# Optimization experiments

Hardware: AMD Instinct MI355X
Metric: run time of the kernel (lower is better)

Reference implementation:

```python
import jax, jax.numpy as jnp
import numpy as np


def setup_inputs() -> dict:
    key = jax.random.key(0)
    B, T = 16384, 768
    inputs = jax.random.normal(key, (B, T, 2), dtype=jnp.float32)
    p = {"capacitance_x": 0.4, "capacitance_y": 0.4}
    for d in ["ax", "by", "xx", "xy", "yx", "yy"]:
        p[f"conductance_{d}"] = 0.001
        p[f"mean_{d}"] = 0.3
        p[f"std_{d}"] = 3.0
        p[f"pot_{d}"] = -1.0 if d in ("xy", "yx") else 1.0
    params = {k: jnp.full((1,), v, dtype=jnp.float32) for k, v in p.items()}
    return {"inputs": inputs, **params}


def reference(inputs, capacitance_x, capacitance_y,
              conductance_ax, mean_ax, std_ax, pot_ax,
              conductance_by, mean_by, std_by, pot_by,
              conductance_xx, mean_xx, std_xx, pot_xx,
              conductance_xy, mean_xy, std_xy, pot_xy,
              conductance_yx, mean_yx, std_yx, pot_yx,
              conductance_yy, mean_yy, std_yy, pot_yy):
    # inputs: [B, T, 2]; scan over T with carried state [B, 2]
    def syn(g, s, m, p, pre, post):
        # conductance * sigmoid(std*(pre-mean)) * (pot - post)
        return g * jax.nn.sigmoid(s * (pre - m)) * (p - post)

    def step(carry, inp):
        x, y = carry[:, :1], carry[:, 1:]          # [B,1] each
        a, b = inp[:, :1], inp[:, 1:]              # [B,1] each
        ix = (syn(conductance_ax, std_ax, mean_ax, pot_ax, a, x)
              + syn(conductance_xx, std_xx, mean_xx, pot_xx, x, x)
              + syn(conductance_yx, std_yx, mean_yx, pot_yx, y, x))
        iy = (syn(conductance_by, std_by, mean_by, pot_by, b, y)
              + syn(conductance_yy, std_yy, mean_yy, pot_yy, y, y)
              + syn(conductance_xy, std_xy, mean_xy, pot_xy, x, y))
        x = x + ix / capacitance_x
        y = y + iy / capacitance_y
        return jnp.concatenate([x, y], axis=-1), x

    B = inputs.shape[0]
    init = jnp.zeros((B, 2), dtype=inputs.dtype)
    _, ys = jax.lax.scan(step, init, jnp.swapaxes(inputs, 0, 1))  # ys: [T,B,1]
    return jnp.swapaxes(ys, 0, 1)  # [B,T,1]
```

## Files before the change

### kernel.cpp

```cpp
#include <hip/hip_runtime.h>

#define T_LEN 768
#define TC 32
#define NCH (T_LEN / TC)
#define RPB 32
#define RS  66
#define OS  66

struct Params { const float* p[27]; };

__device__ __forceinline__ float ex2(float x){ float r; asm("v_exp_f32 %0, %1":"=v"(r):"v"(x)); return r; }
__device__ __forceinline__ float frcp(float x){ return __builtin_amdgcn_rcpf(x); }
__device__ __forceinline__ float dpp_xor1(float x){
    return __int_as_float(__builtin_amdgcn_mov_dpp(__float_as_int(x),0xB1,0xF,0xF,true));
}
__device__ __forceinline__ float psig(float v, float k, float c){
    return frcp(1.0f + ex2(__builtin_fmaf(-k, v, c)));
}
__device__ __forceinline__ void wave_barrier(){
    asm volatile("s_waitcnt lgkmcnt(0)" ::: "memory");
    __builtin_amdgcn_s_barrier();
}

__global__ __launch_bounds__(192, 1) void cell_kernel(Params P, float* __restrict__ out) {
    __shared__ float r1buf[2][TC][RS];
    __shared__ float lds_o[2][TC][OS];

    const int tid = (int)threadIdx.x;
    const int r0  = (int)blockIdx.x * RPB;
    const int wv  = tid >> 6;
    const int l   = tid & 63;

    const float* __restrict__ inp = P.p[0];
    const float capx = P.p[1][0], capy = P.p[2][0];
    const float g_ax = P.p[3][0],  m_ax = P.p[4][0],  s_ax = P.p[5][0],  q_ax = P.p[6][0];
    const float g_by = P.p[7][0],  m_by = P.p[8][0],  s_by = P.p[9][0],  q_by = P.p[10][0];
    const float g_xx = P.p[11][0], m_xx = P.p[12][0], s_xx = P.p[13][0], q_xx = P.p[14][0];
    const float g_xy = P.p[15][0], m_xy = P.p[16][0], s_xy = P.p[17][0], q_xy = P.p[18][0];
    const float g_yx = P.p[19][0], m_yx = P.p[20][0], s_yx = P.p[21][0], q_yx = P.p[22][0];
    const float g_yy = P.p[23][0], m_yy = P.p[24][0], s_yy = P.p[25][0], q_yy = P.p[26][0];

    const float icx = 1.0f / capx, icy = 1.0f / capy;
    const float L2E  = 1.44269504088896340736f;
    const float LN2  = 0.69314718056f;
    const float mLN2 = -0.69314718056f;
    const float mHLN2 = -0.34657359028f;

    const float k1x = s_ax * L2E, c1x = k1x * m_ax;
    const float k1y = s_by * L2E, c1y = k1y * m_by;

    const bool share = (s_yx == s_yy) && (m_yx == m_yy) &&
                       (s_xy == s_xx) && (m_xy == m_xx) &&
                       (s_xx != 0.0f) && (s_yy != 0.0f) &&
                       (g_xx != 0.0f) && (g_yy != 0.0f);

    const float k2xp = s_xx * L2E, c2xp = k2xp * m_xx;
    const float G2xp = g_xx * icx;
    const float A2xp = g_xx * q_xx * icx;
    const float R2xp = __builtin_fmaf(G2xp, c2xp, -k2xp * A2xp);
    const float cv1 = share ? 1.0f / (G2xp * k2xp) : 1.0f;
    const float cv0 = share ? (c2xp / k2xp - R2xp * (1.0f / (G2xp * k2xp))) : 0.0f;

    const float4* __restrict__ in4 = (const float4*)inp;

    if (wv != 0) {
        const int p = wv - 1;
        float4 pinA[4], pinB[4];

        auto LOADP = [&](float4 (&pin)[4], int c) {
            #pragma unroll
            for (int k = 0; k < 4; ++k) { int idx = l + 64*(p*4 + k);
                int r_ = idx >> 4, q = idx & 15;
                pin[k] = in4[(size_t)(r0 + r_) * 384 + c * 16 + q]; }
        };
        auto SIGW = [&](float4 (&pin)[4], int buf) {
            #pragma unroll
            for (int k = 0; k < 4; ++k) { int idx = l + 64*(p*4 + k);
                int r_ = idx >> 4, q = idx & 15;
                float2 w0, w1;
                w0.x = psig(pin[k].x, k1x, c1x);
                w0.y = psig(pin[k].y, k1y, c1y);
                w1.x = psig(pin[k].z, k1x, c1x);
                w1.y = psig(pin[k].w, k1y, c1y);
                *(float2*)&r1buf[buf][2*q]    [2*r_] = w0;
                *(float2*)&r1buf[buf][2*q + 1][2*r_] = w1; }
        };
        auto DRAIN = [&](int c) {
            const int buf = c & 1;
            #pragma unroll
            for (int k = 0; k < 2; ++k) { int f = l + 64*(p*2 + k);
                int r_ = f >> 3, pq = f & 7;
                float4 o;
                o.x = __builtin_fmaf(lds_o[buf][4*pq + 0][2*r_], cv1, cv0);
                o.y = __builtin_fmaf(lds_o[buf][4*pq + 1][2*r_], cv1, cv0);
                o.z = __builtin_fmaf(lds_o[buf][4*pq + 2][2*r_], cv1, cv0);
                o.w = __builtin_fmaf(lds_o[buf][4*pq + 3][2*r_], cv1, cv0);
                *(float4*)&out[(size_t)(r0 + r_) * T_LEN + c * TC + 4*pq] = o; }
        };

        LOADP(pinA, 0);
        LOADP(pinB, 1);
        SIGW(pinA, 0);
        wave_barrier();
        for (int c = 0; c < NCH; ++c) {
            if (c + 2 < NCH) { if ((c & 1) == 0) LOADP(pinA, c + 2);
                               else              LOADP(pinB, c + 2); }
            if (c >= 1) DRAIN(c - 1);
            if (c + 1 < NCH) {
                if ((c & 1) == 0) SIGW(pinB, (c + 1) & 1);
                else              SIGW(pinA, (c + 1) & 1);
            }
            wave_barrier();
        }
        DRAIN(NCH - 1);
    } else {
        __builtin_amdgcn_s_setprio(1);

        const bool isX = (l & 1) == 0;
        const float k2r = (isX ? s_xx : s_yy) * L2E;
        const float c2r = k2r * (isX ? m_xx : m_yy);
        const float k3r = (isX ? s_xy : s_yx) * L2E;
        const float c3r = k3r * (isX ? m_xy : m_yx);
        const float icr = isX ? icx : icy;
        const float A1r = (isX ? g_ax * q_ax : g_by * q_by) * icr, G1r = (isX ? g_ax : g_by) * icr;
        const float A2r = (isX ? g_xx * q_xx : g_yy * q_yy) * icr, G2r = (isX ? g_xx : g_yy) * icr;
        const float A3r = (isX ? g_yx * q_yx : g_xy * q_xy) * icr, G3r = (isX ? g_yx : g_xy) * icr;

        const float R1 = __builtin_fmaf(G1r, c2r, -k2r * A1r);
        const float R2 = __builtin_fmaf(G2r, c2r, -k2r * A2r);
        const float R3 = __builtin_fmaf(G3r, c2r, -k2r * A3r);
        const float mG1 = -G1r, mG2 = -G2r, mG3 = -G3r;
        const float inv_mG2 = 1.0f / mG2;

        float h1 = __builtin_fmaf(mG1, c2r, R1);
        float h2 = __builtin_fmaf(mG2, c2r, R2);
        float h3 = __builtin_fmaf(mG3, c2r, R3);
        float v = 0.0f;

        wave_barrier();
        for (int c = 0; c < NCH; ++c) {
            const int buf = c & 1;
            float rr[TC];
            #pragma unroll
            for (int t = 0; t < TC; ++t) rr[t] = r1buf[buf][t][l];

            if (share) {
                float Wr  = (h2 - R2) * inv_mG2;
                float E   = ex2(Wr);
                float sg  = frcp(1.0f + E);
                float t1  = __builtin_fmaf(-sg, sg, sg);
                float cfac = mLN2 * t1;
                float w2  = __builtin_fmaf(LN2, sg, mHLN2);
                float hd2 = cfac * w2;
                float dl2p = 0.0f;
                float p1 = rr[0] * h1;
                #pragma unroll
                for (int t = 0; t < TC; ++t) {
                    float rp   = dpp_xor1(sg);
                    float s2mW = __builtin_fmaf(sg, h2, p1);
                    float dl   = __builtin_fmaf(rp, h3, s2mW);
                    float inner = __builtin_fmaf(hd2, dl2p, sg);
                    float sgn  = __builtin_fmaf(cfac, dl, inner);
                    dl2p = dl * dl;
                    h1 = __builtin_fmaf(mG1, dl, h1);
                    h2 = __builtin_fmaf(mG2, dl, h2);
                    h3 = __builtin_fmaf(mG3, dl, h3);
                    if (t + 1 < TC) p1 = rr[t + 1] * h1;
                    t1   = __builtin_fmaf(-sgn, sgn, sgn);
                    cfac = mLN2 * t1;
                    if ((t & 3) == 3) {
                        w2  = __builtin_fmaf(LN2, sgn, mHLN2);
                        hd2 = cfac * w2;
                    }
                    lds_o[buf][t][l] = h2;
                    sg = sgn;
                }
            } else {
                #pragma unroll
                for (int t = 0; t < TC; ++t) {
                    float s2 = psig(v, k2r, c2r);
                    float s3 = psig(v, k3r, c3r);
                    float rp = dpp_xor1(s3);
                    float u1 = __builtin_fmaf(-v, G1r, A1r);
                    float u2 = __builtin_fmaf(-v, G2r, A2r);
                    float u3 = __builtin_fmaf(-v, G3r, A3r);
                    v = __builtin_fmaf(rp, u3,
                        __builtin_fmaf(s2, u2,
                        __builtin_fmaf(rr[t], u1, v)));
                    lds_o[buf][t][l] = v;
                }
            }
            wave_barrier();
        }
    }
}

extern "C" void kernel_launch(void* const* d_in, const int* in_sizes, int n_in,
                              void* d_out, int out_size, void* d_ws, size_t ws_size,
                              hipStream_t stream) {
    (void)d_ws; (void)ws_size; (void)out_size; (void)n_in;
    Params P;
    for (int i = 0; i < 27; ++i) P.p[i] = (const float*)d_in[i];
    float* out = (float*)d_out;
    const int B = in_sizes[0] / (T_LEN * 2);
    dim3 grid(B / RPB);
    cell_kernel<<<grid, dim3(192), 0, stream>>>(P, out);
}
```

Before: 35.36 us.

## Process chunk pairs per barrier and prefetch next chunk's inputs during serial scan

Groups two time chunks into a super-chunk so producer and consumer waves meet at a barrier half as often, and grows the LDS ring buffers from 2 to 4 slots. In the shared-parameter path, the serial wave loads the second chunk's sigmoid inputs from LDS while computing the first chunk, which hides LDS latency inside the dependent recurrence. Producer waves now load and transform 8 float4s per stage, which raises register pressure. The input buffer row stride also changes from 66 to 67 to alter the LDS bank mapping.

```diff
diff --git a/kernel.cpp b/kernel.cpp
--- a/kernel.cpp
+++ b/kernel.cpp
@@ -3,8 +3,9 @@
 #define T_LEN 768
 #define TC 32
 #define NCH (T_LEN / TC)
+#define NSUP (NCH / 2)
 #define RPB 32
-#define RS  66
+#define RS  67
 #define OS  66
 
 struct Params { const float* p[27]; };
@@ -22,9 +23,50 @@
     __builtin_amdgcn_s_barrier();
 }
 
+template<bool PREF>
+__device__ __forceinline__ void serial_share(
+    int l, const float* r1nxt, float* ocur,
+    const float (&rr)[TC], float (&rrN)[TC],
+    float& h1, float& h2, float& h3,
+    float mG1, float mG2, float mG3, float R2, float inv_mG2)
+{
+    const float LN2 = 0.69314718056f, mLN2 = -0.69314718056f, mHLN2 = -0.34657359028f;
+    float Wr  = (h2 - R2) * inv_mG2;
+    float E   = ex2(Wr);
+    float sg  = frcp(1.0f + E);
+    float t1  = __builtin_fmaf(-sg, sg, sg);
+    float cfac = mLN2 * t1;
+    float w2  = __builtin_fmaf(LN2, sg, mHLN2);
+    float hd2 = cfac * w2;
+    float dl2p = 0.0f;
+    float p1 = rr[0] * h1;
+    #pragma unroll
+    for (int t = 0; t < TC; ++t) {
+        if constexpr (PREF) rrN[t] = r1nxt[t * RS + l];
+        float rp   = dpp_xor1(sg);
+        float s2mW = __builtin_fmaf(sg, h2, p1);
+        float dl   = __builtin_fmaf(rp, h3, s2mW);
+        float inner = __builtin_fmaf(hd2, dl2p, sg);
+        float sgn  = __builtin_fmaf(cfac, dl, inner);
+        dl2p = dl * dl;
+        h1 = __builtin_fmaf(mG1, dl, h1);
+        h2 = __builtin_fmaf(mG2, dl, h2);
+        h3 = __builtin_fmaf(mG3, dl, h3);
+        if (t + 1 < TC) p1 = rr[t + 1] * h1;
+        t1   = __builtin_fmaf(-sgn, sgn, sgn);
+        cfac = mLN2 * t1;
+        if ((t & 3) == 3) {
+            w2  = __builtin_fmaf(LN2, sgn, mHLN2);
+            hd2 = cfac * w2;
+        }
+        ocur[t * OS + l] = h2;
+        sg = sgn;
+    }
+}
+
 __global__ __launch_bounds__(192, 1) void cell_kernel(Params P, float* __restrict__ out) {
-    __shared__ float r1buf[2][TC][RS];
-    __shared__ float lds_o[2][TC][OS];
+    __shared__ float r1buf[4][TC][RS];
+    __shared__ float lds_o[4][TC][OS];
 
     const int tid = (int)threadIdx.x;
     const int r0  = (int)blockIdx.x * RPB;
@@ -42,9 +84,6 @@
 
     const float icx = 1.0f / capx, icy = 1.0f / capy;
     const float L2E  = 1.44269504088896340736f;
-    const float LN2  = 0.69314718056f;
-    const float mLN2 = -0.69314718056f;
-    const float mHLN2 = -0.34657359028f;
 
     const float k1x = s_ax * L2E, c1x = k1x * m_ax;
     const float k1y = s_by * L2E, c1y = k1y * m_by;
@@ -65,17 +104,21 @@
 
     if (wv != 0) {
         const int p = wv - 1;
-        float4 pinA[4], pinB[4];
-
-        auto LOADP = [&](float4 (&pin)[4], int c) {
-            #pragma unroll
-            for (int k = 0; k < 4; ++k) { int idx = l + 64*(p*4 + k);
+        float4 pinA[8], pinB[8];
+
+        auto LOADPAIR = [&](float4 (&pin)[8], int sp) {
+            #pragma unroll
+            for (int k = 0; k < 8; ++k) {
+                int idx = l + 64 * (p * 4 + (k & 3));
+                int ch  = 2 * sp + (k >> 2);
                 int r_ = idx >> 4, q = idx & 15;
-                pin[k] = in4[(size_t)(r0 + r_) * 384 + c * 16 + q]; }
+                pin[k] = in4[(size_t)(r0 + r_) * 384 + ch * 16 + q]; }
         };
-        auto SIGW = [&](float4 (&pin)[4], int buf) {
-            #pragma unroll
-            for (int k = 0; k < 4; ++k) { int idx = l + 64*(p*4 + k);
+        auto SIGPAIR = [&](float4 (&pin)[8], int sp) {
+            #pragma unroll
+            for (int k = 0; k < 8; ++k) {
+                int idx = l + 64 * (p * 4 + (k & 3));
+                int buf = (2 * sp + (k >> 2)) & 3;
                 int r_ = idx >> 4, q = idx & 15;
                 float2 w0, w1;
                 w0.x = psig(pin[k].x, k1x, c1x);
@@ -85,10 +128,11 @@
                 *(float2*)&r1buf[buf][2*q]    [2*r_] = w0;
                 *(float2*)&r1buf[buf][2*q + 1][2*r_] = w1; }
         };
-        auto DRAIN = [&](int c) {
-            const int buf = c & 1;
-            #pragma unroll
-            for (int k = 0; k < 2; ++k) { int f = l + 64*(p*2 + k);
+        auto DRAINC = [&](int c) {
+            const int buf = c & 3;
+            #pragma unroll
+            for (int k = 0; k < 2; ++k) {
+                int f = l + 64 * (p * 2 + k);
                 int r_ = f >> 3, pq = f & 7;
                 float4 o;
                 o.x = __builtin_fmaf(lds_o[buf][4*pq + 0][2*r_], cv1, cv0);
@@ -98,21 +142,23 @@
                 *(float4*)&out[(size_t)(r0 + r_) * T_LEN + c * TC + 4*pq] = o; }
         };
 
-        LOADP(pinA, 0);
-        LOADP(pinB, 1);
-        SIGW(pinA, 0);
+        LOADPAIR(pinA, 0);
+        LOADPAIR(pinB, 1);
+        SIGPAIR(pinA, 0);
         wave_barrier();
-        for (int c = 0; c < NCH; ++c) {
-            if (c + 2 < NCH) { if ((c & 1) == 0) LOADP(pinA, c + 2);
-                               else              LOADP(pinB, c + 2); }
-            if (c >= 1) DRAIN(c - 1);
-            if (c + 1 < NCH) {
-                if ((c & 1) == 0) SIGW(pinB, (c + 1) & 1);
-                else              SIGW(pinA, (c + 1) & 1);
+        for (int s = 0; s < NSUP; ++s) {
+            if (s + 2 < NSUP) {
+                if ((s & 1) == 0) LOADPAIR(pinA, s + 2);
+                else              LOADPAIR(pinB, s + 2);
+            }
+            if (s >= 1) { DRAINC(2*s - 2); DRAINC(2*s - 1); }
+            if (s + 1 < NSUP) {
+                if ((s & 1) == 0) SIGPAIR(pinB, s + 1);
+                else              SIGPAIR(pinA, s + 1);
             }
             wave_barrier();
         }
-        DRAIN(NCH - 1);
+        DRAINC(NCH - 2); DRAINC(NCH - 1);
     } else {
         __builtin_amdgcn_s_setprio(1);
 
@@ -138,44 +184,29 @@
         float v = 0.0f;
 
         wave_barrier();
-        for (int c = 0; c < NCH; ++c) {
-            const int buf = c & 1;
-            float rr[TC];
-            #pragma unroll
-            for (int t = 0; t < TC; ++t) rr[t] = r1buf[buf][t][l];
-
-            if (share) {
-                float Wr  = (h2 - R2) * inv_mG2;
-                float E   = ex2(Wr);
-                float sg  = frcp(1.0f + E);
-                float t1  = __builtin_fmaf(-sg, sg, sg);
-                float cfac = mLN2 * t1;
-                float w2  = __builtin_fmaf(LN2, sg, mHLN2);
-                float hd2 = cfac * w2;
-                float dl2p = 0.0f;
-                float p1 = rr[0] * h1;
+        if (share) {
+            float rrA[TC], rrB[TC];
+            #pragma unroll
+            for (int t = 0; t < TC; ++t) rrA[t] = r1buf[0][t][l];
+            for (int s = 0; s < NSUP; ++s) {
+                const int s0 = (2*s) & 3, s1 = (2*s + 1) & 3;
+                serial_share<true >(l, &r1buf[s1][0][0], &lds_o[s0][0][0],
+                                    rrA, rrB, h1, h2, h3, mG1, mG2, mG3, R2, inv_mG2);
+                serial_share<false>(l, &r1buf[s1][0][0], &lds_o[s1][0][0],
+                                    rrB, rrA, h1, h2, h3, mG1, mG2, mG3, R2, inv_mG2);
+                wave_barrier();
+                if (s + 1 < NSUP) {
+                    const int sn = (2*s + 2) & 3;
+                    #pragma unroll
+                    for (int t = 0; t < TC; ++t) rrA[t] = r1buf[sn][t][l];
+                }
+            }
+        } else {
+            for (int c = 0; c < NCH; ++c) {
+                const int buf = c & 3;
+                float rr[TC];
                 #pragma unroll
-                for (int t = 0; t < TC; ++t) {
-                    float rp   = dpp_xor1(sg);
-                    float s2mW = __builtin_fmaf(sg, h2, p1);
-                    float dl   = __builtin_fmaf(rp, h3, s2mW);
-                    float inner = __builtin_fmaf(hd2, dl2p, sg);
-                    float sgn  = __builtin_fmaf(cfac, dl, inner);
-                    dl2p = dl * dl;
-                    h1 = __builtin_fmaf(mG1, dl, h1);
-                    h2 = __builtin_fmaf(mG2, dl, h2);
-                    h3 = __builtin_fmaf(mG3, dl, h3);
-                    if (t + 1 < TC) p1 = rr[t + 1] * h1;
-                    t1   = __builtin_fmaf(-sgn, sgn, sgn);
-                    cfac = mLN2 * t1;
-                    if ((t & 3) == 3) {
-                        w2  = __builtin_fmaf(LN2, sgn, mHLN2);
-                        hd2 = cfac * w2;
-                    }
-                    lds_o[buf][t][l] = h2;
-                    sg = sgn;
-                }
-            } else {
+                for (int t = 0; t < TC; ++t) rr[t] = r1buf[buf][t][l];
                 #pragma unroll
                 for (int t = 0; t < TC; ++t) {
                     float s2 = psig(v, k2r, c2r);
@@ -189,8 +220,8 @@
                         __builtin_fmaf(rr[t], u1, v)));
                     lds_o[buf][t][l] = v;
                 }
-            }
-            wave_barrier();
+                if (c & 1) wave_barrier();
+            }
         }
     }
 }
```

New measurement: 35.86 us. Within noise of the previous version (+1.4%).
